# Optimization experiments

Measured on AMD Instinct MI355X. Metric: run time of the kernel, lower is better.

## Reference

```python
import jax, jax.numpy as jnp
import numpy as np

D_MODEL = 1024
H = 16
DK = D_MODEL // H
S = 4096


def setup_inputs() -> dict:
    key = jax.random.key(0)
    ks = jax.random.split(key, 11)
    scale = 1.0 / np.sqrt(D_MODEL)
    return {
        "Q": jax.random.normal(ks[0], (S, D_MODEL), jnp.float32),
        "K": jax.random.normal(ks[1], (S, D_MODEL), jnp.float32),
        "V": jax.random.normal(ks[2], (S, D_MODEL), jnp.float32),
        # per-head projection weights, stacked: [h, d_model, d_k]
        "Wq": jax.random.normal(ks[3], (H, D_MODEL, DK), jnp.float32) * scale,
        "bq": jax.random.normal(ks[4], (H, DK), jnp.float32) * 0.01,
        "Wk": jax.random.normal(ks[5], (H, D_MODEL, DK), jnp.float32) * scale,
        "bk": jax.random.normal(ks[6], (H, DK), jnp.float32) * 0.01,
        "Wv": jax.random.normal(ks[7], (H, D_MODEL, DK), jnp.float32) * scale,
        "bv": jax.random.normal(ks[8], (H, DK), jnp.float32) * 0.01,
        # output projection (torch Linear convention: y = x @ Wo.T + bo)
        "Wo": jax.random.normal(ks[9], (D_MODEL, D_MODEL), jnp.float32) * scale,
        "bo": jax.random.normal(ks[10], (D_MODEL,), jnp.float32) * 0.01,
    }


def reference(Q, K, V, Wq, bq, Wk, bk, Wv, bv, Wo, bo):
    # per-head projections, vectorized over heads: [h, S, d_k]
    q = jnp.einsum("sd,hdk->hsk", Q, Wq) + bq[:, None, :]
    k = jnp.einsum("sd,hdk->hsk", K, Wk) + bk[:, None, :]
    v = jnp.einsum("sd,hdk->hsk", V, Wv) + bv[:, None, :]
    # scaled dot-product attention (full [h, S, S] scores, as in the original)
    scores = jnp.einsum("hsk,htk->hst", q, k) / jnp.sqrt(jnp.float32(DK))
    attn = jax.nn.softmax(scores, axis=-1)
    o = jnp.einsum("hst,htk->hsk", attn, v)
    # concat heads along feature dim: [S, h*d_k]
    x = jnp.transpose(o, (1, 0, 2)).reshape(S, D_MODEL)
    return x @ Wo.T + bo
```

## Files before the change

### kernel.cpp

```cpp
#include <hip/hip_runtime.h>

typedef unsigned short u16;
typedef unsigned int u32;
using f32x4 = __attribute__((ext_vector_type(4))) float;
using f32x16 = __attribute__((ext_vector_type(16))) float;
using u32x4 = __attribute__((ext_vector_type(4))) u32;
using bf16x8 = __attribute__((ext_vector_type(8))) __bf16;

#define DEV __device__ __forceinline__

DEV u16 f2bf(float f) {
  u32 x = __builtin_bit_cast(u32, f);
  return (u16)((x + 0x7fffu + ((x >> 16) & 1u)) >> 16);
}

DEV f32x4 mfma16(bf16x8 a, bf16x8 b, f32x4 c) {
  return __builtin_amdgcn_mfma_f32_16x16x32_bf16(a, b, c, 0, 0, 0);
}
DEV f32x16 mfma32(bf16x8 a, bf16x8 b, f32x16 c) {
  return __builtin_amdgcn_mfma_f32_32x32x16_bf16(a, b, c, 0, 0, 0);
}

DEV float ex2(float x) {
#if __has_builtin(__builtin_amdgcn_exp2f)
  return __builtin_amdgcn_exp2f(x);
#else
  float r;
  asm("v_exp_f32 %0, %1" : "=v"(r) : "v"(x));
  return r;
#endif
}

DEV int swz(int row, int byteInRow) {
  return row * 128 + ((((byteInRow >> 4) ^ (row & 7)) << 4) | (byteInRow & 15));
}

DEV u32 pkbf(float lo, float hi) {
  union { u32 u; __bf16 h[2]; } x;
  x.h[0] = (__bf16)lo; x.h[1] = (__bf16)hi;
  return x.u;
}

DEV void gload16(const u16* g, u16* l) {
  __builtin_amdgcn_global_load_lds((const __attribute__((address_space(1))) void*)g,
                                   (__attribute__((address_space(3))) void*)l, 16, 0, 0);
}

__global__ __launch_bounds__(256) void prep_kernel(
    const float* __restrict__ Q, const float* __restrict__ K, const float* __restrict__ V,
    const float* __restrict__ Wo, const float* __restrict__ Wq, const float* __restrict__ Wk,
    const float* __restrict__ Wv, u16* __restrict__ Qb, u16* __restrict__ Kb,
    u16* __restrict__ Vb, u16* __restrict__ Wob, u16* __restrict__ Tq, u16* __restrict__ Tk,
    u16* __restrict__ Tv) {
  __shared__ u16 t[64][68];
  int y = blockIdx.y, tid = threadIdx.x;
  if (y < 4) {
    if (y == 3 && blockIdx.x >= 1024) return;
    const float* in = y == 0 ? Q : y == 1 ? K : y == 2 ? V : Wo;
    u16* out = y == 0 ? Qb : y == 1 ? Kb : y == 2 ? Vb : Wob;
    int i = blockIdx.x * 256 + tid;
    float4 v = ((const float4*)in)[i];
    ushort4 w;
    w.x = f2bf(v.x); w.y = f2bf(v.y); w.z = f2bf(v.z); w.w = f2bf(v.w);
    ((ushort4*)out)[i] = w;
    return;
  }
  if (blockIdx.x >= 768) return;
  int which = blockIdx.x >> 8, h = (blockIdx.x >> 4) & 15, d0 = (blockIdx.x & 15) * 64;
  const float* W = which == 0 ? Wq : (which == 1 ? Wk : Wv);
  u16* T = which == 0 ? Tq : (which == 1 ? Tk : Tv);
#pragma unroll
  for (int i = 0; i < 4; ++i) {
    int c = i * 256 + tid;
    int r = c >> 4, c4 = (c & 15) * 4;
    float4 v = *(const float4*)(W + h * 65536 + (d0 + r) * 64 + c4);
    t[r][c4] = f2bf(v.x); t[r][c4 + 1] = f2bf(v.y);
    t[r][c4 + 2] = f2bf(v.z); t[r][c4 + 3] = f2bf(v.w);
  }
  __syncthreads();
#pragma unroll
  for (int i = 0; i < 4; ++i) {
    int ch = i * 256 + tid;
    int cc = ch >> 4, d4 = (ch & 15) * 4;
    ushort4 w;
    w.x = t[d4][cc]; w.y = t[d4 + 1][cc]; w.z = t[d4 + 2][cc]; w.w = t[d4 + 3][cc];
    *(ushort4*)(T + (h * 64 + cc) * 1024 + d0 + d4) = w;
  }
}

__global__ __launch_bounds__(256, 3) void gemm_qkv(
    const u16* __restrict__ Qb, const u16* __restrict__ Kb, const u16* __restrict__ Vb,
    const u16* __restrict__ Tq, const u16* __restrict__ Tk, const u16* __restrict__ Tv,
    const float* __restrict__ bq, const float* __restrict__ bk, const float* __restrict__ bv,
    u16* __restrict__ qh, u16* __restrict__ kh, u16* __restrict__ vTh, float sc) {
  __shared__ alignas(16) u16 lA[128 * 64];
  __shared__ alignas(16) u16 lB[128 * 64];
  int z = blockIdx.z;
  const u16* A = z == 0 ? Qb : z == 1 ? Kb : Vb;
  const u16* B = z == 0 ? Tq : z == 1 ? Tk : Tv;
  const float* bias = z == 0 ? bq : z == 1 ? bk : bv;
  int bm = blockIdx.x, bn = blockIdx.y;
  const char* gA = (const char*)(A + bm * 131072);
  const char* gB = (const char*)(B + bn * 131072);
  int tid = threadIdx.x;
  int wid = tid >> 6, lane = tid & 63, g = lane >> 4, ln = lane & 15;
  int wr = wid >> 1, wc = wid & 1;
  const char* sA[4]; const char* sB[4];
  u16* dA[4]; u16* dB[4];
#pragma unroll
  for (int i = 0; i < 4; ++i) {
    int c = i * 256 + tid, row = c >> 3, cc = c & 7;
    int sw = (cc ^ (row & 7)) << 4;
    sA[i] = gA + row * 2048 + sw;
    sB[i] = gB + row * 2048 + sw;
    dA[i] = (u16*)((char*)lA + i * 4096 + wid * 1024);
    dB[i] = (u16*)((char*)lB + i * 4096 + wid * 1024);
  }
  f32x4 acc[4][4] = {};
  for (int k0 = 0; k0 < 1024; k0 += 64) {
#pragma unroll
    for (int i = 0; i < 4; ++i) {
      gload16((const u16*)(sA[i] + k0 * 2), dA[i]);
      gload16((const u16*)(sB[i] + k0 * 2), dB[i]);
    }
    __syncthreads();
#pragma unroll
    for (int ks = 0; ks < 2; ++ks) {
      bf16x8 af[4], bfr[4];
#pragma unroll
      for (int mt = 0; mt < 4; ++mt) {
        int row = wr * 64 + mt * 16 + ln;
        af[mt] = *(const bf16x8*)((const char*)lA + swz(row, ks * 64 + g * 16));
      }
#pragma unroll
      for (int nt = 0; nt < 4; ++nt) {
        int row = wc * 64 + nt * 16 + ln;
        bfr[nt] = *(const bf16x8*)((const char*)lB + swz(row, ks * 64 + g * 16));
      }
#pragma unroll
      for (int mt = 0; mt < 4; ++mt)
#pragma unroll
        for (int nt = 0; nt < 4; ++nt)
          acc[mt][nt] = mfma16(af[mt], bfr[nt], acc[mt][nt]);
    }
    __syncthreads();
  }
  float scale = z == 0 ? sc : 1.f;
  float bv_[4];
#pragma unroll
  for (int nt = 0; nt < 4; ++nt) bv_[nt] = bias[bn * 128 + wc * 64 + nt * 16 + ln];
  if (z < 2) {
    u16* out = z == 0 ? qh : kh;
#pragma unroll
    for (int mt = 0; mt < 4; ++mt)
      for (int nt = 0; nt < 4; ++nt)
        for (int r = 0; r < 4; ++r) {
          int s = bm * 128 + wr * 64 + mt * 16 + g * 4 + r;
          int j = bn * 128 + wc * 64 + nt * 16 + ln;
          out[(j >> 6) * 262144 + s * 64 + (j & 63)] = f2bf((acc[mt][nt][r] + bv_[nt]) * scale);
        }
  } else {
#pragma unroll
    for (int mt = 0; mt < 4; ++mt)
      for (int nt = 0; nt < 4; ++nt) {
        int sb = bm * 128 + wr * 64 + mt * 16 + g * 4;
        int j = bn * 128 + wc * 64 + nt * 16 + ln;
        ushort4 w;
        w.x = f2bf(acc[mt][nt][0] + bv_[nt]);
        w.y = f2bf(acc[mt][nt][1] + bv_[nt]);
        w.z = f2bf(acc[mt][nt][2] + bv_[nt]);
        w.w = f2bf(acc[mt][nt][3] + bv_[nt]);
        *(ushort4*)(vTh + j * 4096 + sb) = w;
      }
  }
}

__global__ __launch_bounds__(256) void gemm_out(const u16* __restrict__ A,
                                                const u16* __restrict__ B,
                                                const float* __restrict__ bias,
                                                float* __restrict__ out) {
  __shared__ alignas(16) u16 lA[64 * 64];
  __shared__ alignas(16) u16 lB[128 * 64];
  int tid = threadIdx.x;
  int wid = tid >> 6, lane = tid & 63, g = lane >> 4, ln = lane & 15;
  int wr = wid >> 1, wc = wid & 1;
  int bm = blockIdx.x, bn = blockIdx.y;
  const char* gA = (const char*)(A + bm * 65536);
  const char* gB = (const char*)(B + bn * 131072);
  const char* sA[2]; const char* sB[4];
  u16* dA[2]; u16* dB[4];
#pragma unroll
  for (int i = 0; i < 4; ++i) {
    int c = i * 256 + tid, row = c >> 3, cc = c & 7;
    int sw = (cc ^ (row & 7)) << 4;
    if (i < 2) {
      sA[i] = gA + row * 2048 + sw;
      dA[i] = (u16*)((char*)lA + i * 4096 + wid * 1024);
    }
    sB[i] = gB + row * 2048 + sw;
    dB[i] = (u16*)((char*)lB + i * 4096 + wid * 1024);
  }
  f32x4 acc[2][4] = {};
  for (int k0 = 0; k0 < 1024; k0 += 64) {
#pragma unroll
    for (int i = 0; i < 2; ++i) gload16((const u16*)(sA[i] + k0 * 2), dA[i]);
#pragma unroll
    for (int i = 0; i < 4; ++i) gload16((const u16*)(sB[i] + k0 * 2), dB[i]);
    __syncthreads();
#pragma unroll
    for (int ks = 0; ks < 2; ++ks) {
      bf16x8 af[2], bfr[4];
#pragma unroll
      for (int mt = 0; mt < 2; ++mt) {
        int row = wr * 32 + mt * 16 + ln;
        af[mt] = *(const bf16x8*)((const char*)lA + swz(row, ks * 64 + g * 16));
      }
#pragma unroll
      for (int nt = 0; nt < 4; ++nt) {
        int row = wc * 64 + nt * 16 + ln;
        bfr[nt] = *(const bf16x8*)((const char*)lB + swz(row, ks * 64 + g * 16));
      }
#pragma unroll
      for (int mt = 0; mt < 2; ++mt)
#pragma unroll
        for (int nt = 0; nt < 4; ++nt)
          acc[mt][nt] = mfma16(af[mt], bfr[nt], acc[mt][nt]);
    }
    __syncthreads();
  }
  float bv_[4];
#pragma unroll
  for (int nt = 0; nt < 4; ++nt) bv_[nt] = bias[bn * 128 + wc * 64 + nt * 16 + ln];
#pragma unroll
  for (int mt = 0; mt < 2; ++mt)
    for (int nt = 0; nt < 4; ++nt)
      for (int r = 0; r < 4; ++r) {
        int s = bm * 64 + wr * 32 + mt * 16 + g * 4 + r;
        int j = bn * 128 + wc * 64 + nt * 16 + ln;
        out[s * 1024 + j] = acc[mt][nt][r] + bv_[nt];
      }
}

__global__ __launch_bounds__(512, 4) void flash_attn2(const u16* __restrict__ qh,
                                                      const u16* __restrict__ kh,
                                                      const u16* __restrict__ vT,
                                                      u16* __restrict__ x) {
  __shared__ alignas(16) char smem[66560];
  u16* lK = (u16*)smem;
  u16* lV = (u16*)(smem + 32768);
  float* lbuf = (float*)(smem + 65536);
  float* mergeBuf = (float*)smem;

  int tid = threadIdx.x;
  int wid = tid >> 6, lane = tid & 63;
  int grp = wid >> 2, sw = wid & 3;
  int lq = lane & 31, hi = lane >> 5;
  int nb = (blockIdx.x & 7) * 64 + (blockIdx.x >> 3);
  int h = nb >> 5, qt = nb & 31;

  const u16* gK = kh + h * 262144 + grp * 131072;
  const u16* gV = vT + h * 262144 + grp * 2048;
  u16* lKg = lK + grp * 8192;
  u16* lVg = lV + grp * 8192;

  bf16x8 qf[4];
  {
    const u16* gQ = qh + h * 262144 + (qt * 128 + sw * 32 + lq) * 64 + hi * 8;
#pragma unroll
    for (int st = 0; st < 4; ++st) qf[st] = *(const bf16x8*)(gQ + st * 16);
  }
  f32x16 o0 = {}, o1 = {};
  float l_run = 0.f;

  int r8 = lane >> 3, pc = lane & 7;
  int rowA = sw * 16 + r8, rowB = rowA + 8;
  const u16* pKA = gK + rowA * 64 + ((pc ^ (rowA & 7)) << 3);
  const u16* pKB = gK + rowB * 64 + ((pc ^ (rowB & 7)) << 3);
  const u16* pVA = gV + rowA * 4096 + ((pc ^ (rowA & 7)) << 3);
  const u16* pVB = gV + rowB * 4096 + ((pc ^ (rowB & 7)) << 3);
  u16* dKA = lKg + (sw * 16) * 64;
  u16* dKB = dKA + 512;
  u16* dVA = lVg + (sw * 16) * 64;
  u16* dVB = dVA + 512;

  gload16(pKA, dKA); gload16(pKB, dKB);
  gload16(pVA, dVA); gload16(pVB, dVB);
  pKA += 4096; pKB += 4096;
  pVA += 64; pVB += 64;

  const int NT = 32;
  for (int t = 0; t < NT; ++t) {
    asm volatile("s_waitcnt vmcnt(0)" ::: "memory");
    __builtin_amdgcn_s_barrier();
    __builtin_amdgcn_sched_barrier(0);
    int cur = t & 1;
    if (t + 1 < NT) {
      int nxt = (cur ^ 1) * 4096;
      gload16(pKA, dKA + nxt); gload16(pKB, dKB + nxt);
      gload16(pVA, dVA + nxt); gload16(pVB, dVB + nxt);
      pKA += 4096; pKB += 4096; pVA += 64; pVB += 64;
    }
    const u16* lKc = lKg + cur * 4096;
    const u16* lVc = lVg + cur * 4096;
    f32x16 s0 = {}, s1 = {};
    __builtin_amdgcn_s_setprio(1);
#pragma unroll
    for (int st = 0; st < 4; ++st) {
      bf16x8 k0 = *(const bf16x8*)((const char*)lKc + swz(lq, st * 32 + hi * 16));
      bf16x8 k1 = *(const bf16x8*)((const char*)lKc + swz(32 + lq, st * 32 + hi * 16));
      s0 = mfma32(k0, qf[st], s0);
      s1 = mfma32(k1, qf[st], s1);
    }
    __builtin_amdgcn_s_setprio(0);
#pragma unroll
    for (int r = 0; r < 16; ++r) {
      s0[r] = ex2(s0[r]);
      s1[r] = ex2(s1[r]);
    }
    float c0 = s0[0] + s1[0], c1 = s0[1] + s1[1];
    float c2 = s0[2] + s1[2], c3 = s0[3] + s1[3];
#pragma unroll
    for (int r = 4; r < 16; r += 4) {
      c0 += s0[r] + s1[r];
      c1 += s0[r + 1] + s1[r + 1];
      c2 += s0[r + 2] + s1[r + 2];
      c3 += s0[r + 3] + s1[r + 3];
    }
    float sm = (c0 + c1) + (c2 + c3);
    l_run += sm + __shfl_xor(sm, 32);
    bf16x8 pa[4];
#pragma unroll
    for (int n = 0; n < 2; ++n)
#pragma unroll
      for (int b2 = 0; b2 < 2; ++b2) {
        int b = b2 * 8;
        u32x4 wv;
        if (n == 0) {
          wv[0] = pkbf(s0[b + 0], s0[b + 1]); wv[1] = pkbf(s0[b + 2], s0[b + 3]);
          wv[2] = pkbf(s0[b + 4], s0[b + 5]); wv[3] = pkbf(s0[b + 6], s0[b + 7]);
        } else {
          wv[0] = pkbf(s1[b + 0], s1[b + 1]); wv[1] = pkbf(s1[b + 2], s1[b + 3]);
          wv[2] = pkbf(s1[b + 4], s1[b + 5]); wv[3] = pkbf(s1[b + 6], s1[b + 7]);
        }
        pa[n * 2 + b2] = __builtin_bit_cast(bf16x8, wv);
      }
    __builtin_amdgcn_s_setprio(1);
#pragma unroll
    for (int st = 0; st < 4; ++st) {
      uint2 a0 = *(const uint2*)((const char*)lVc + swz(lq, st * 32 + hi * 8));
      uint2 a1 = *(const uint2*)((const char*)lVc + swz(lq, st * 32 + 16 + hi * 8));
      uint2 b0 = *(const uint2*)((const char*)lVc + swz(32 + lq, st * 32 + hi * 8));
      uint2 b1 = *(const uint2*)((const char*)lVc + swz(32 + lq, st * 32 + 16 + hi * 8));
      u32x4 w0; w0[0] = a0.x; w0[1] = a0.y; w0[2] = a1.x; w0[3] = a1.y;
      u32x4 w1; w1[0] = b0.x; w1[1] = b0.y; w1[2] = b1.x; w1[3] = b1.y;
      o0 = mfma32(pa[st], __builtin_bit_cast(bf16x8, w0), o0);
      o1 = mfma32(pa[st], __builtin_bit_cast(bf16x8, w1), o1);
    }
    __builtin_amdgcn_s_setprio(0);
  }

  if (hi == 0) lbuf[grp * 128 + sw * 32 + lq] = l_run;
  __syncthreads();
  if (grp == 1) {
#pragma unroll
    for (int r = 0; r < 16; ++r) {
      int rq = (r & 3) + 8 * (r >> 2) + 4 * hi;
      float* mb = mergeBuf + (sw * 32 + rq) * 64;
      mb[lq] = o0[r];
      mb[32 + lq] = o1[r];
    }
  }
  __syncthreads();
  if (grp == 0) {
#pragma unroll
    for (int r = 0; r < 16; ++r) {
      int rq = (r & 3) + 8 * (r >> 2) + 4 * hi;
      float inv = 1.f / (lbuf[sw * 32 + rq] + lbuf[128 + sw * 32 + rq]);
      const float* mb = mergeBuf + (sw * 32 + rq) * 64;
      int srow = qt * 128 + sw * 32 + rq;
      u16* xr = x + srow * 1024 + h * 64;
      xr[lq] = f2bf((o0[r] + mb[lq]) * inv);
      xr[32 + lq] = f2bf((o1[r] + mb[32 + lq]) * inv);
    }
  }
}

extern "C" void kernel_launch(void* const* d_in, const int* in_sizes, int n_in,
                              void* d_out, int out_size, void* d_ws, size_t ws_size,
                              hipStream_t stream) {
  (void)in_sizes; (void)n_in; (void)out_size; (void)ws_size;
  const float* Q  = (const float*)d_in[0];
  const float* K  = (const float*)d_in[1];
  const float* V  = (const float*)d_in[2];
  const float* Wq = (const float*)d_in[3];
  const float* bq = (const float*)d_in[4];
  const float* Wk = (const float*)d_in[5];
  const float* bk = (const float*)d_in[6];
  const float* Wv = (const float*)d_in[7];
  const float* bv = (const float*)d_in[8];
  const float* Wo = (const float*)d_in[9];
  const float* bo = (const float*)d_in[10];

  char* ws = (char*)d_ws;
  u16* Qb  = (u16*)(ws + (0ull << 20));
  u16* Kb  = (u16*)(ws + (8ull << 20));
  u16* Vb  = (u16*)(ws + (16ull << 20));
  u16* Tq  = (u16*)(ws + (24ull << 20));
  u16* Tk  = (u16*)(ws + (26ull << 20));
  u16* Tv  = (u16*)(ws + (28ull << 20));
  u16* Wob = (u16*)(ws + (30ull << 20));
  u16* qh  = (u16*)(ws + (32ull << 20));
  u16* kh  = (u16*)(ws + (40ull << 20));
  u16* vTh = (u16*)(ws + (48ull << 20));
  u16* xb  = (u16*)(ws + (56ull << 20));

  const float SC = 0.125f * 1.44269504089f;

  prep_kernel<<<dim3(4096, 5), 256, 0, stream>>>(Q, K, V, Wo, Wq, Wk, Wv,
                                                 Qb, Kb, Vb, Wob, Tq, Tk, Tv);

  gemm_qkv<<<dim3(32, 8, 3), 256, 0, stream>>>(Qb, Kb, Vb, Tq, Tk, Tv, bq, bk, bv,
                                               qh, kh, vTh, SC);

  flash_attn2<<<512, 512, 0, stream>>>(qh, kh, vTh, xb);

  gemm_out<<<dim3(64, 8), 256, 0, stream>>>(xb, Wob, bo, (float*)d_out);
}
```

Baseline: 153.3 us.

## Fuse fp32-to-bf16 activation conversion into QKV projection GEMM

Drops the separate pass that converted Q, K, V from fp32 to bf16. The QKV GEMM now loads the fp32 activation tiles straight into LDS with a 16-way XOR swizzle and packs them to bf16 while reading fragments. This removes a full read-write pass over roughly 48MB of activations and shrinks the prep kernel grid. The cost is that each A tile is now read as fp32 eight times, once per bn block, and LDS use doubles for A, which may lower occupancy.

```diff
diff --git a/kernel.cpp b/kernel.cpp
--- a/kernel.cpp
+++ b/kernel.cpp
@@ -47,22 +47,18 @@
 }
 
 __global__ __launch_bounds__(256) void prep_kernel(
-    const float* __restrict__ Q, const float* __restrict__ K, const float* __restrict__ V,
-    const float* __restrict__ Wo, const float* __restrict__ Wq, const float* __restrict__ Wk,
-    const float* __restrict__ Wv, u16* __restrict__ Qb, u16* __restrict__ Kb,
-    u16* __restrict__ Vb, u16* __restrict__ Wob, u16* __restrict__ Tq, u16* __restrict__ Tk,
+    const float* __restrict__ Wo, const float* __restrict__ Wq,
+    const float* __restrict__ Wk, const float* __restrict__ Wv,
+    u16* __restrict__ Wob, u16* __restrict__ Tq, u16* __restrict__ Tk,
     u16* __restrict__ Tv) {
   __shared__ u16 t[64][68];
   int y = blockIdx.y, tid = threadIdx.x;
-  if (y < 4) {
-    if (y == 3 && blockIdx.x >= 1024) return;
-    const float* in = y == 0 ? Q : y == 1 ? K : y == 2 ? V : Wo;
-    u16* out = y == 0 ? Qb : y == 1 ? Kb : y == 2 ? Vb : Wob;
+  if (y == 0) {
     int i = blockIdx.x * 256 + tid;
-    float4 v = ((const float4*)in)[i];
+    float4 v = ((const float4*)Wo)[i];
     ushort4 w;
     w.x = f2bf(v.x); w.y = f2bf(v.y); w.z = f2bf(v.z); w.w = f2bf(v.w);
-    ((ushort4*)out)[i] = w;
+    ((ushort4*)Wob)[i] = w;
     return;
   }
   if (blockIdx.x >= 768) return;
@@ -89,48 +85,60 @@
 }
 
 __global__ __launch_bounds__(256, 3) void gemm_qkv(
-    const u16* __restrict__ Qb, const u16* __restrict__ Kb, const u16* __restrict__ Vb,
+    const float* __restrict__ Qf, const float* __restrict__ Kf, const float* __restrict__ Vf,
     const u16* __restrict__ Tq, const u16* __restrict__ Tk, const u16* __restrict__ Tv,
     const float* __restrict__ bq, const float* __restrict__ bk, const float* __restrict__ bv,
     u16* __restrict__ qh, u16* __restrict__ kh, u16* __restrict__ vTh, float sc) {
-  __shared__ alignas(16) u16 lA[128 * 64];
+  __shared__ alignas(16) float lAf[128 * 64];
   __shared__ alignas(16) u16 lB[128 * 64];
   int z = blockIdx.z;
-  const u16* A = z == 0 ? Qb : z == 1 ? Kb : Vb;
+  const float* Af = z == 0 ? Qf : z == 1 ? Kf : Vf;
   const u16* B = z == 0 ? Tq : z == 1 ? Tk : Tv;
   const float* bias = z == 0 ? bq : z == 1 ? bk : bv;
   int bm = blockIdx.x, bn = blockIdx.y;
-  const char* gA = (const char*)(A + bm * 131072);
+  const char* gA = (const char*)(Af + bm * 131072);
   const char* gB = (const char*)(B + bn * 131072);
   int tid = threadIdx.x;
   int wid = tid >> 6, lane = tid & 63, g = lane >> 4, ln = lane & 15;
   int wr = wid >> 1, wc = wid & 1;
-  const char* sA[4]; const char* sB[4];
-  u16* dA[4]; u16* dB[4];
+  const char* sA[8];
+  u16* dA[8];
+#pragma unroll
+  for (int i = 0; i < 8; ++i) {
+    int c2 = i * 256 + tid, row = c2 >> 4, p = c2 & 15;
+    sA[i] = gA + row * 4096 + ((p ^ (row & 15)) << 4);
+    dA[i] = (u16*)((char*)lAf + i * 4096 + wid * 1024);
+  }
+  const char* sB[4];
+  u16* dB[4];
 #pragma unroll
   for (int i = 0; i < 4; ++i) {
     int c = i * 256 + tid, row = c >> 3, cc = c & 7;
     int sw = (cc ^ (row & 7)) << 4;
-    sA[i] = gA + row * 2048 + sw;
     sB[i] = gB + row * 2048 + sw;
-    dA[i] = (u16*)((char*)lA + i * 4096 + wid * 1024);
     dB[i] = (u16*)((char*)lB + i * 4096 + wid * 1024);
   }
   f32x4 acc[4][4] = {};
   for (int k0 = 0; k0 < 1024; k0 += 64) {
 #pragma unroll
-    for (int i = 0; i < 4; ++i) {
-      gload16((const u16*)(sA[i] + k0 * 2), dA[i]);
-      gload16((const u16*)(sB[i] + k0 * 2), dB[i]);
-    }
+    for (int i = 0; i < 4; ++i) gload16((const u16*)(sB[i] + k0 * 2), dB[i]);
+#pragma unroll
+    for (int i = 0; i < 8; ++i) gload16((const u16*)(sA[i] + k0 * 4), dA[i]);
     __syncthreads();
 #pragma unroll
     for (int ks = 0; ks < 2; ++ks) {
       bf16x8 af[4], bfr[4];
 #pragma unroll
       for (int mt = 0; mt < 4; ++mt) {
-        int row = wr * 64 + mt * 16 + ln;
-        af[mt] = *(const bf16x8*)((const char*)lA + swz(row, ks * 64 + g * 16));
+        int r = wr * 64 + mt * 16 + ln;
+        const char* rowp = (const char*)lAf + r * 256;
+        int c0 = ks * 8 + g * 2;
+        f32x4 fa = *(const f32x4*)(rowp + ((c0 ^ (r & 15)) << 4));
+        f32x4 fb = *(const f32x4*)(rowp + (((c0 + 1) ^ (r & 15)) << 4));
+        u32x4 w;
+        w[0] = pkbf(fa[0], fa[1]); w[1] = pkbf(fa[2], fa[3]);
+        w[2] = pkbf(fb[0], fb[1]); w[3] = pkbf(fb[2], fb[3]);
+        af[mt] = __builtin_bit_cast(bf16x8, w);
       }
 #pragma unroll
       for (int nt = 0; nt < 4; ++nt) {
@@ -402,9 +410,6 @@
   const float* bo = (const float*)d_in[10];
 
   char* ws = (char*)d_ws;
-  u16* Qb  = (u16*)(ws + (0ull << 20));
-  u16* Kb  = (u16*)(ws + (8ull << 20));
-  u16* Vb  = (u16*)(ws + (16ull << 20));
   u16* Tq  = (u16*)(ws + (24ull << 20));
   u16* Tk  = (u16*)(ws + (26ull << 20));
   u16* Tv  = (u16*)(ws + (28ull << 20));
@@ -416,10 +421,9 @@
 
   const float SC = 0.125f * 1.44269504089f;
 
-  prep_kernel<<<dim3(4096, 5), 256, 0, stream>>>(Q, K, V, Wo, Wq, Wk, Wv,
-                                                 Qb, Kb, Vb, Wob, Tq, Tk, Tv);
-
-  gemm_qkv<<<dim3(32, 8, 3), 256, 0, stream>>>(Qb, Kb, Vb, Tq, Tk, Tv, bq, bk, bv,
+  prep_kernel<<<dim3(1024, 2), 256, 0, stream>>>(Wo, Wq, Wk, Wv, Wob, Tq, Tk, Tv);
+
+  gemm_qkv<<<dim3(32, 8, 3), 256, 0, stream>>>(Q, K, V, Tq, Tk, Tv, bq, bk, bv,
                                                qh, kh, vTh, SC);
 
   flash_attn2<<<512, 512, 0, stream>>>(qh, kh, vTh, xb);
```

New measurement: 154.9 us. About the same (+1.1%).
